# Performance work log

Hardware: AMD Instinct MI355X
Metric: run time of the kernel (lower is better)

The kernel has to match this reference:

```python
import jax, jax.numpy as jnp
import numpy as np

B, S, E, H = 4, 2048, 1024, 16
D = E // H  # head dim = 64


def setup_inputs() -> dict:
    key = jax.random.key(0)
    ks = jax.random.split(key, 5)
    s = 0.02
    return {
        "x": jax.random.normal(ks[0], (B, S, E), dtype=jnp.float32),
        "Wq": jax.random.normal(ks[1], (E, E), dtype=jnp.float32) * s,
        "Wk": jax.random.normal(ks[2], (E, E), dtype=jnp.float32) * s,
        "Wv": jax.random.normal(ks[3], (E, E), dtype=jnp.float32) * s,
        "Wo": jax.random.normal(ks[4], (E, E), dtype=jnp.float32) * s,
        "bo": jnp.zeros((E,), dtype=jnp.float32),
    }


def reference(x, Wq, Wk, Wv, Wo, bo):
    b, s, e = x.shape
    h, d = H, e // H
    # QKV projections -> [b, h, s, d]
    q = (x @ Wq).reshape(b, s, h, d).transpose(0, 2, 1, 3)
    k = (x @ Wk).reshape(b, s, h, d).transpose(0, 2, 1, 3)
    v = (x @ Wv).reshape(b, s, h, d).transpose(0, 2, 1, 3)
    # scores [b, h, s, s], causal mask with -inf, scaled softmax
    a = jnp.einsum('bhqd,bhkd->bhqk', q, k)
    causal = jnp.tril(jnp.ones((s, s), dtype=bool))  # True where allowed
    a = jnp.where(causal, a, -jnp.inf) / jnp.sqrt(jnp.asarray(d, x.dtype))
    a = jax.nn.softmax(a, axis=-1)
    # dropout p=0.0 (identity in eval)
    y = jnp.einsum('bhqk,bhkd->bhqd', a, v)
    y = y.transpose(0, 2, 1, 3).reshape(b, s, e)
    return y @ Wo + bo
```

## Files before the change

### kernel.cpp

```cpp
#include <hip/hip_runtime.h>

typedef __bf16 bf16x8 __attribute__((ext_vector_type(8)));
typedef float f32x4 __attribute__((ext_vector_type(4)));
typedef unsigned short u16x8 __attribute__((ext_vector_type(8)));

#define S_LEN 2048
#define NHEAD 16
#define HDIM  64
#define EMB   1024

__device__ __forceinline__ ushort f2b(float v) {
  union { float f; unsigned u; } x; x.f = v;
  unsigned r = (x.u + 0x7fffu + ((x.u >> 16) & 1u)) >> 16;
  return (ushort)r;
}

__device__ __forceinline__ ushort f2b_trunc(float v) {
  union { float f; unsigned u; } x; x.f = v;
  return (ushort)(x.u >> 16);
}

typedef const __attribute__((address_space(1))) unsigned int* gp1_t;
typedef __attribute__((address_space(3))) unsigned int* lp3_t;
__device__ __forceinline__ void gld16(const ushort* g, const ushort* l) {
  __builtin_amdgcn_global_load_lds((gp1_t)(unsigned long long)(uintptr_t)g,
                                   (lp3_t)(unsigned int)(uintptr_t)l, 16, 0, 0);
}

__device__ __forceinline__ void barf() {
  asm volatile("" ::: "memory");
  __builtin_amdgcn_s_barrier();
  asm volatile("" ::: "memory");
}

__global__ __launch_bounds__(256) void prep_kernel(
    const float* __restrict__ x, const float* __restrict__ W0,
    const float* __restrict__ W1, const float* __restrict__ W2,
    const float* __restrict__ W3, ushort* __restrict__ xb,
    ushort* __restrict__ Wt0, ushort* __restrict__ Wt1,
    ushort* __restrict__ Wt2, ushort* __restrict__ Wt3, float scale0) {
  const int z = blockIdx.z;
  if (z == 4) {
    size_t base = ((size_t)(blockIdx.y * 32 + blockIdx.x)) * 8192 + threadIdx.x * 4;
#pragma unroll
    for (int i = 0; i < 8; ++i) {
      float4 v = *(const float4*)(x + base + i * 1024);
      ushort4 o;
      o.x = f2b(v.x); o.y = f2b(v.y); o.z = f2b(v.z); o.w = f2b(v.w);
      *(ushort4*)(xb + base + i * 1024) = o;
    }
    return;
  }
  __shared__ float t[32][33];
  const float* W = z == 0 ? W0 : (z == 1 ? W1 : (z == 2 ? W2 : W3));
  ushort* Wt = z == 0 ? Wt0 : (z == 1 ? Wt1 : (z == 2 ? Wt2 : Wt3));
  const float scale = z == 0 ? scale0 : 1.0f;
  int k0 = blockIdx.x * 32, n0 = blockIdx.y * 32;
  int c = threadIdx.x & 31, r0 = threadIdx.x >> 5;
#pragma unroll
  for (int i = 0; i < 4; ++i) {
    int r = r0 + i * 8;
    t[r][c] = W[(size_t)(k0 + r) * EMB + n0 + c];
  }
  __syncthreads();
#pragma unroll
  for (int i = 0; i < 4; ++i) {
    int r = r0 + i * 8;
    Wt[(size_t)(n0 + r) * EMB + k0 + c] = f2b(t[c][r] * scale);
  }
}

template <int EPI>
__global__ __launch_bounds__(512, 2) void gemm8_kernel(
    const ushort* __restrict__ A, const ushort* __restrict__ Bt,
    ushort* __restrict__ outQ, ushort* __restrict__ outK, ushort* __restrict__ outVt,
    float* __restrict__ outF, const float* __restrict__ bias) {
  __shared__ ushort lds8[73728];
  const int tid = threadIdx.x;
  const int wave = tid >> 6, lane = tid & 63, ln = lane & 15, quad = lane >> 4;
  const int wm = wave >> 2, wn = wave & 3;
  const long m0 = (long)blockIdx.x * 128, n0 = (long)blockIdx.y * 256;
  constexpr int K = EMB, KT = K / 64;

  const int srow = tid >> 3;
  const int scol = ((tid & 7) ^ (srow & 7)) * 8;
  const ushort* srcA = A + (m0 + srow) * (long)K + scol;
  const ushort* srcB = Bt + (n0 + srow) * (long)K + scol;

#define STG_A(t, s)                                                            \
  do {                                                                         \
    gld16(srcA + (t) * 64,               lds8 + (s) * 8192 + tid * 8);         \
    gld16(srcA + (t) * 64 + 64 * K,      lds8 + (s) * 8192 + 4096 + tid * 8);  \
  } while (0)
#define STG_B(t, s)                                                            \
  do {                                                                         \
    gld16(srcB + (t) * 64,               lds8 + 24576 + (s) * 16384 + tid * 8);         \
    gld16(srcB + (t) * 64 + 64 * K,      lds8 + 24576 + (s) * 16384 + 4096 + tid * 8);  \
    gld16(srcB + (t) * 64 + 128 * K,     lds8 + 24576 + (s) * 16384 + 8192 + tid * 8);  \
    gld16(srcB + (t) * 64 + 192 * K,     lds8 + 24576 + (s) * 16384 + 12288 + tid * 8); \
  } while (0)

  const int sw = (ln & 7) * 8;

#define RD_A(F, kk, s)                                                         \
  do {                                                                         \
    const ushort* p_ = lds8 + (s) * 8192 + (wm * 64 + ln) * 64 +               \
                       (((kk) * 32 + quad * 8) ^ sw);                          \
    F[0] = *(const bf16x8*)p_;                                                 \
    F[1] = *(const bf16x8*)(p_ + 1024);                                        \
    F[2] = *(const bf16x8*)(p_ + 2048);                                        \
    F[3] = *(const bf16x8*)(p_ + 3072);                                        \
  } while (0)
#define RD_B(F, kk, s)                                                         \
  do {                                                                         \
    const ushort* p_ = lds8 + 24576 + (s) * 16384 + (wn * 64 + ln) * 64 +      \
                       (((kk) * 32 + quad * 8) ^ sw);                          \
    F[0] = *(const bf16x8*)p_;                                                 \
    F[1] = *(const bf16x8*)(p_ + 1024);                                        \
    F[2] = *(const bf16x8*)(p_ + 2048);                                        \
    F[3] = *(const bf16x8*)(p_ + 3072);                                        \
  } while (0)

#define MM16(AF, BF)                                                           \
  do {                                                                         \
    __builtin_amdgcn_s_setprio(1);                                             \
    _Pragma("unroll") for (int mt = 0; mt < 4; ++mt)                           \
        _Pragma("unroll") for (int nt = 0; nt < 4; ++nt)                       \
            acc[mt][nt] = __builtin_amdgcn_mfma_f32_16x16x32_bf16(             \
                AF[mt], BF[nt], acc[mt][nt], 0, 0, 0);                         \
    __builtin_amdgcn_s_setprio(0);                                             \
  } while (0)

  f32x4 acc[4][4] = {};
  bf16x8 afP[4], bfP[4], afN[4], bfN[4];

  STG_A(0, 0); STG_B(0, 0);
  STG_A(1, 1); STG_B(1, 1);
  asm volatile("s_waitcnt vmcnt(6)" ::: "memory");
  barf();
  RD_A(afP, 0, 0); RD_B(bfP, 0, 0);

#define TILE_FULL(t, s, s1, s2)                                                \
  do {                                                                         \
    STG_A((t) + 2, s2);                                                        \
    RD_A(afN, 1, s); RD_B(bfN, 1, s);                                          \
    MM16(afP, bfP);                               \
    STG_B((t) + 2, s2);                                                        \
    asm volatile("s_waitcnt vmcnt(6) lgkmcnt(0)" ::: "memory");                \
    barf();                               \
    RD_A(afP, 0, s1); RD_B(bfP, 0, s1);                        \
    MM16(afN, bfN);                               \
  } while (0)

  for (int th = 0; th < 12; th += 3) {
    TILE_FULL(th, 0, 1, 2);
    TILE_FULL(th + 1, 1, 2, 0);
    TILE_FULL(th + 2, 2, 0, 1);
  }
  TILE_FULL(12, 0, 1, 2);
  TILE_FULL(13, 1, 2, 0);
  RD_A(afN, 1, 2); RD_B(bfN, 1, 2);
  MM16(afP, bfP);
  asm volatile("s_waitcnt vmcnt(0) lgkmcnt(0)" ::: "memory");
  barf();
  RD_A(afP, 0, 0); RD_B(bfP, 0, 0);
  MM16(afN, bfN);
  RD_A(afN, 1, 0); RD_B(bfN, 1, 0);
  MM16(afP, bfP);
  MM16(afN, bfN);

  if (EPI == 0) {
    const int sel = (int)(n0 >> 10);
    if (sel == 2) {
#pragma unroll
      for (int mt = 0; mt < 4; ++mt) {
        const long mbase = m0 + wm * 64 + mt * 16 + quad * 4;
        const long bb = mbase >> 11, s = mbase & 2047;
#pragma unroll
        for (int nt = 0; nt < 4; ++nt) {
          const int nn = (int)((n0 & 1023) + wn * 64 + nt * 16 + ln);
          const int h = nn >> 6, d = nn & 63;
          uint2 val;
          val.x = (unsigned)f2b(acc[mt][nt][0]) | ((unsigned)f2b(acc[mt][nt][1]) << 16);
          val.y = (unsigned)f2b(acc[mt][nt][2]) | ((unsigned)f2b(acc[mt][nt][3]) << 16);
          *(uint2*)(outVt + (((bb * NHEAD + h) * (long)HDIM + d) * S_LEN) + s) = val;
        }
      }
    } else {
      ushort* dst = sel == 0 ? outQ : outK;
#pragma unroll
      for (int mt = 0; mt < 4; ++mt) {
#pragma unroll
        for (int nt = 0; nt < 4; ++nt) {
          const int nn = (int)((n0 & 1023) + wn * 64 + nt * 16 + ln);
          const int h = nn >> 6, d = nn & 63;
#pragma unroll
          for (int r = 0; r < 4; ++r) {
            const long m = m0 + wm * 64 + mt * 16 + quad * 4 + r;
            const long bb = m >> 11, s = m & 2047;
            dst[(((bb * NHEAD + h) * S_LEN) + s) * HDIM + d] = f2b(acc[mt][nt][r]);
          }
        }
      }
    }
  } else {
#pragma unroll
    for (int mt = 0; mt < 4; ++mt) {
#pragma unroll
      for (int nt = 0; nt < 4; ++nt) {
        const long n = n0 + wn * 64 + nt * 16 + ln;
        const float bv = bias[n];
#pragma unroll
        for (int r = 0; r < 4; ++r) {
          const long m = m0 + wm * 64 + mt * 16 + quad * 4 + r;
          outF[m * (long)EMB + n] = acc[mt][nt][r] + bv;
        }
      }
    }
  }
#undef TILE_FULL
#undef MM16
#undef RD_B
#undef RD_A
#undef STG_B
#undef STG_A
}

__global__ __launch_bounds__(256) void attn_kernel(const ushort* __restrict__ Q,
                                                   const ushort* __restrict__ Kg,
                                                   const ushort* __restrict__ Vt,
                                                   ushort* __restrict__ Y) {
  __shared__ alignas(16) ushort Ks[2][4096];
  __shared__ alignas(16) ushort Vs[2][4096];
  __shared__ alignas(16) ushort Ps[4 * 2 * 16 * 72];
  const int tid = threadIdx.x;
  const int wave = tid >> 6, lane = tid & 63, ln = lane & 15, quad = lane >> 4;
  const int bh = blockIdx.x;
  const int qb = 15 - (int)blockIdx.y;
  const int q0 = qb * 128;
  const size_t base = (size_t)bh * S_LEN * HDIM;
  const int ntiles = 2 * qb + 2;

  const u16x8 ob = {0x3F80, 0x3F80, 0x3F80, 0x3F80, 0x3F80, 0x3F80, 0x3F80, 0x3F80};
  const bf16x8 ones = __builtin_bit_cast(bf16x8, ob);

  bf16x8 qf[2][2];
#pragma unroll
  for (int mt = 0; mt < 2; ++mt)
#pragma unroll
    for (int ks2 = 0; ks2 < 2; ++ks2)
      qf[mt][ks2] = *(const bf16x8*)(Q + base + (size_t)(q0 + wave * 32 + mt * 16 + ln) * HDIM +
                                     ks2 * 32 + quad * 8);

  f32x4 acc[2][4] = {};
  f32x4 accl[2] = {};

  const int srow = tid >> 3;
  const int scc  = ((tid & 7) ^ (srow & 7)) * 8;
  const ushort* KgS = Kg + base + (size_t)srow * HDIM + scc;
  const ushort* VgS = Vt + base + (size_t)srow * S_LEN + scc;

  {
    gld16(KgS,                       &Ks[0][0] + tid * 8);
    gld16(KgS + 32 * HDIM,           &Ks[0][0] + 2048 + tid * 8);
    gld16(VgS,                       &Vs[0][0] + tid * 8);
    gld16(VgS + 32 * (size_t)S_LEN,  &Vs[0][0] + 2048 + tid * 8);
  }
  __syncthreads();

  ushort* Pw0 = Ps + wave * 2304;
  ushort* Pw1 = Pw0 + 1152;
  const int swW = (quad >> 1) << 4;
  const int swR = (ln >> 3) << 4;
  const int swL = (ln & 7) * 8;

  for (int kt = 0; kt < ntiles; ++kt) {
    const int cur = kt & 1;
    const int k0 = kt * 64;
    if (kt + 1 < ntiles) {
      const int nb = cur ^ 1;
      const size_t k1 = (size_t)(k0 + 64);
      gld16(KgS + k1 * HDIM,                  &Ks[nb][0] + tid * 8);
      gld16(KgS + (k1 + 32) * HDIM,           &Ks[nb][0] + 2048 + tid * 8);
      gld16(VgS + k1,                         &Vs[nb][0] + tid * 8);
      gld16(VgS + 32 * (size_t)S_LEN + k1,    &Vs[nb][0] + 2048 + tid * 8);
    }
    const ushort* Kc = &Ks[cur][0];
    const ushort* Vc = &Vs[cur][0];
    const int qbase = q0 + wave * 32;

    if (k0 < qbase + 32) {
      f32x4 s0[4] = {}, s1[4] = {};
#pragma unroll
      for (int ks2 = 0; ks2 < 2; ++ks2) {
#pragma unroll
        for (int nt = 0; nt < 4; ++nt) {
          bf16x8 bk = *(const bf16x8*)(Kc + (nt * 16 + ln) * 64 +
                                       ((ks2 * 32 + quad * 8) ^ swL));
          s0[nt] = __builtin_amdgcn_mfma_f32_16x16x32_bf16(qf[0][ks2], bk, s0[nt], 0, 0, 0);
          s1[nt] = __builtin_amdgcn_mfma_f32_16x16x32_bf16(qf[1][ks2], bk, s1[nt], 0, 0, 0);
        }
      }

      if (k0 + 63 > qbase) {
        const int rowq = qbase + quad * 4;
#pragma unroll
        for (int nt = 0; nt < 4; ++nt)
#pragma unroll
          for (int r = 0; r < 4; ++r) {
            const int key = k0 + nt * 16 + ln;
            if (key > rowq + r) s0[nt][r] = -3.0e38f;
            if (key > rowq + 16 + r) s1[nt][r] = -3.0e38f;
          }
      }

      asm volatile("" ::: "memory");
#pragma unroll
      for (int nt = 0; nt < 4; ++nt) {
#pragma unroll
        for (int r = 0; r < 4; ++r) {
          float p0 = __builtin_amdgcn_exp2f(s0[nt][r]);
          float p1 = __builtin_amdgcn_exp2f(s1[nt][r]);
          const int row = (quad * 4 + r) * 72;
          const int col = (nt * 16 + ln) ^ swW;
          Pw0[row + col] = f2b_trunc(p0);
          Pw1[row + col] = f2b_trunc(p1);
        }
      }
      asm volatile("" ::: "memory");

#pragma unroll
      for (int ks2 = 0; ks2 < 2; ++ks2) {
        const int rcol = (ks2 * 32 + quad * 8) ^ swR;
        bf16x8 ap0 = *(const bf16x8*)(Pw0 + ln * 72 + rcol);
        bf16x8 ap1 = *(const bf16x8*)(Pw1 + ln * 72 + rcol);
        accl[0] = __builtin_amdgcn_mfma_f32_16x16x32_bf16(ap0, ones, accl[0], 0, 0, 0);
        accl[1] = __builtin_amdgcn_mfma_f32_16x16x32_bf16(ap1, ones, accl[1], 0, 0, 0);
#pragma unroll
        for (int t2 = 0; t2 < 4; ++t2) {
          bf16x8 bv = *(const bf16x8*)(Vc + (t2 * 16 + ln) * 64 +
                                       ((ks2 * 32 + quad * 8) ^ swL));
          acc[0][t2] = __builtin_amdgcn_mfma_f32_16x16x32_bf16(ap0, bv, acc[0][t2], 0, 0, 0);
          acc[1][t2] = __builtin_amdgcn_mfma_f32_16x16x32_bf16(ap1, bv, acc[1][t2], 0, 0, 0);
        }
      }
    }
    __syncthreads();
  }

  const long b = bh >> 4;
  const int h = bh & 15;
#pragma unroll
  for (int mt = 0; mt < 2; ++mt) {
#pragma unroll
    for (int r = 0; r < 4; ++r) {
      float inv = 1.0f / accl[mt][r];
      const int qq = q0 + wave * 32 + mt * 16 + quad * 4 + r;
#pragma unroll
      for (int t2 = 0; t2 < 4; ++t2)
        Y[(((b * S_LEN + qq) * NHEAD) + h) * HDIM + t2 * 16 + ln] = f2b(acc[mt][t2][r] * inv);
    }
  }
}

extern "C" void kernel_launch(void* const* d_in, const int* in_sizes, int n_in,
                              void* d_out, int out_size, void* d_ws, size_t ws_size,
                              hipStream_t stream) {
  const float* x  = (const float*)d_in[0];
  const float* Wq = (const float*)d_in[1];
  const float* Wk = (const float*)d_in[2];
  const float* Wv = (const float*)d_in[3];
  const float* Wo = (const float*)d_in[4];
  const float* bo = (const float*)d_in[5];
  float* out = (float*)d_out;

  const size_t XE = (size_t)8192 * EMB;
  ushort* ws    = (ushort*)d_ws;
  ushort* xb    = ws;
  ushort* Wtqkv = xb + XE;
  ushort* Wto   = Wtqkv + 3 * 1048576;
  ushort* Qb    = Wto + 1048576;
  ushort* Kb    = Qb + XE;
  ushort* Vtb   = Kb + XE;
  ushort* Yb    = xb;

  const float SCALE_Q = 1.4426950408889634f / 8.0f;

  prep_kernel<<<dim3(32, 32, 5), 256, 0, stream>>>(
      x, Wq, Wk, Wv, Wo, xb, Wtqkv, Wtqkv + 1048576, Wtqkv + 2097152, Wto, SCALE_Q);

  gemm8_kernel<0><<<dim3(64, 12), 512, 0, stream>>>(xb, Wtqkv, Qb, Kb, Vtb,
                                                    nullptr, nullptr);
  attn_kernel<<<dim3(64, 16), 256, 0, stream>>>(Qb, Kb, Vtb, Yb);
  gemm8_kernel<1><<<dim3(64, 4), 512, 0, stream>>>(Yb, Wto, nullptr, nullptr,
                                                   nullptr, out, bo);
}
```

Before: 233.9 us.

## Use 32x32x16 MFMA with transposed scores and register-shuffled P, dropping LDS staging

Rewrites the attention inner loop to use 32x32x16 bf16 MFMAs. Scores are computed transposed (K as the A operand), so each lane holds probabilities that can be packed into bf16 pairs and exchanged between half-waves with __shfl_xor to form the A operand for the PV product. This removes the per-tile LDS write/read round trip for P and its shared buffer, and launch bounds now request 3 blocks per CU. In exchange it adds cross-lane shuffles and selects, and puts more pressure on registers.

```diff
diff --git a/kernel.cpp b/kernel.cpp
--- a/kernel.cpp
+++ b/kernel.cpp
@@ -2,7 +2,9 @@
 
 typedef __bf16 bf16x8 __attribute__((ext_vector_type(8)));
 typedef float f32x4 __attribute__((ext_vector_type(4)));
+typedef float f32x16 __attribute__((ext_vector_type(16)));
 typedef unsigned short u16x8 __attribute__((ext_vector_type(8)));
+typedef unsigned int u32x4 __attribute__((ext_vector_type(4)));
 
 #define S_LEN 2048
 #define NHEAD 16
@@ -18,6 +20,11 @@
 __device__ __forceinline__ ushort f2b_trunc(float v) {
   union { float f; unsigned u; } x; x.f = v;
   return (ushort)(x.u >> 16);
+}
+
+__device__ __forceinline__ unsigned pk2(float lo, float hi) {
+  union { float f; unsigned u; } a, b; a.f = lo; b.f = hi;
+  return (b.u & 0xffff0000u) | (a.u >> 16);
 }
 
 typedef const __attribute__((address_space(1))) unsigned int* gp1_t;
@@ -144,12 +151,12 @@
   do {                                                                         \
     STG_A((t) + 2, s2);                                                        \
     RD_A(afN, 1, s); RD_B(bfN, 1, s);                                          \
-    MM16(afP, bfP);                               \
+    MM16(afP, bfP);                                                            \
     STG_B((t) + 2, s2);                                                        \
     asm volatile("s_waitcnt vmcnt(6) lgkmcnt(0)" ::: "memory");                \
-    barf();                               \
-    RD_A(afP, 0, s1); RD_B(bfP, 0, s1);                        \
-    MM16(afN, bfN);                               \
+    barf();                                                                    \
+    RD_A(afP, 0, s1); RD_B(bfP, 0, s1);                                        \
+    MM16(afN, bfN);                                                            \
   } while (0)
 
   for (int th = 0; th < 12; th += 3) {
@@ -226,15 +233,15 @@
 #undef STG_A
 }
 
-__global__ __launch_bounds__(256) void attn_kernel(const ushort* __restrict__ Q,
-                                                   const ushort* __restrict__ Kg,
-                                                   const ushort* __restrict__ Vt,
-                                                   ushort* __restrict__ Y) {
+__global__ __launch_bounds__(256, 3) void attn_kernel(const ushort* __restrict__ Q,
+                                                      const ushort* __restrict__ Kg,
+                                                      const ushort* __restrict__ Vt,
+                                                      ushort* __restrict__ Y) {
   __shared__ alignas(16) ushort Ks[2][4096];
   __shared__ alignas(16) ushort Vs[2][4096];
-  __shared__ alignas(16) ushort Ps[4 * 2 * 16 * 72];
   const int tid = threadIdx.x;
-  const int wave = tid >> 6, lane = tid & 63, ln = lane & 15, quad = lane >> 4;
+  const int wave = tid >> 6, lane = tid & 63;
+  const int l31 = lane & 31, hi = lane >> 5;
   const int bh = blockIdx.x;
   const int qb = 15 - (int)blockIdx.y;
   const int q0 = qb * 128;
@@ -244,16 +251,13 @@
   const u16x8 ob = {0x3F80, 0x3F80, 0x3F80, 0x3F80, 0x3F80, 0x3F80, 0x3F80, 0x3F80};
   const bf16x8 ones = __builtin_bit_cast(bf16x8, ob);
 
-  bf16x8 qf[2][2];
-#pragma unroll
-  for (int mt = 0; mt < 2; ++mt)
-#pragma unroll
-    for (int ks2 = 0; ks2 < 2; ++ks2)
-      qf[mt][ks2] = *(const bf16x8*)(Q + base + (size_t)(q0 + wave * 32 + mt * 16 + ln) * HDIM +
-                                     ks2 * 32 + quad * 8);
-
-  f32x4 acc[2][4] = {};
-  f32x4 accl[2] = {};
+  bf16x8 qf[4];
+#pragma unroll
+  for (int dsub = 0; dsub < 4; ++dsub)
+    qf[dsub] = *(const bf16x8*)(Q + base + (size_t)(q0 + wave * 32 + l31) * HDIM +
+                                dsub * 16 + hi * 8);
+
+  f32x16 acc0 = {}, acc1 = {}, accl = {};
 
   const int srow = tid >> 3;
   const int scc  = ((tid & 7) ^ (srow & 7)) * 8;
@@ -268,11 +272,8 @@
   }
   __syncthreads();
 
-  ushort* Pw0 = Ps + wave * 2304;
-  ushort* Pw1 = Pw0 + 1152;
-  const int swW = (quad >> 1) << 4;
-  const int swR = (ln >> 3) << 4;
-  const int swL = (ln & 7) * 8;
+  const int swL = (lane & 7) * 8;
+  const int qbase = q0 + wave * 32;
 
   for (int kt = 0; kt < ntiles; ++kt) {
     const int cur = kt & 1;
@@ -287,63 +288,69 @@
     }
     const ushort* Kc = &Ks[cur][0];
     const ushort* Vc = &Vs[cur][0];
-    const int qbase = q0 + wave * 32;
 
     if (k0 < qbase + 32) {
-      f32x4 s0[4] = {}, s1[4] = {};
-#pragma unroll
-      for (int ks2 = 0; ks2 < 2; ++ks2) {
-#pragma unroll
-        for (int nt = 0; nt < 4; ++nt) {
-          bf16x8 bk = *(const bf16x8*)(Kc + (nt * 16 + ln) * 64 +
-                                       ((ks2 * 32 + quad * 8) ^ swL));
-          s0[nt] = __builtin_amdgcn_mfma_f32_16x16x32_bf16(qf[0][ks2], bk, s0[nt], 0, 0, 0);
-          s1[nt] = __builtin_amdgcn_mfma_f32_16x16x32_bf16(qf[1][ks2], bk, s1[nt], 0, 0, 0);
+      f32x16 sT0 = {}, sT1 = {};
+#pragma unroll
+      for (int dsub = 0; dsub < 4; ++dsub) {
+        const int c = (dsub * 16 + hi * 8) ^ swL;
+        bf16x8 kf0 = *(const bf16x8*)(Kc + l31 * 64 + c);
+        bf16x8 kf1 = *(const bf16x8*)(Kc + (32 + l31) * 64 + c);
+        sT0 = __builtin_amdgcn_mfma_f32_32x32x16_bf16(kf0, qf[dsub], sT0, 0, 0, 0);
+        sT1 = __builtin_amdgcn_mfma_f32_32x32x16_bf16(kf1, qf[dsub], sT1, 0, 0, 0);
+      }
+
+      if (k0 + 63 > qbase) {
+        const int rowq = qbase + l31;
+#pragma unroll
+        for (int r = 0; r < 16; ++r) {
+          const int key = k0 + ((r & 3) + 8 * (r >> 2)) + 4 * hi;
+          if (key > rowq) sT0[r] = -3.0e38f;
+          if (key + 32 > rowq) sT1[r] = -3.0e38f;
         }
       }
 
-      if (k0 + 63 > qbase) {
-        const int rowq = qbase + quad * 4;
-#pragma unroll
-        for (int nt = 0; nt < 4; ++nt)
-#pragma unroll
-          for (int r = 0; r < 4; ++r) {
-            const int key = k0 + nt * 16 + ln;
-            if (key > rowq + r) s0[nt][r] = -3.0e38f;
-            if (key > rowq + 16 + r) s1[nt][r] = -3.0e38f;
-          }
-      }
-
-      asm volatile("" ::: "memory");
-#pragma unroll
-      for (int nt = 0; nt < 4; ++nt) {
-#pragma unroll
-        for (int r = 0; r < 4; ++r) {
-          float p0 = __builtin_amdgcn_exp2f(s0[nt][r]);
-          float p1 = __builtin_amdgcn_exp2f(s1[nt][r]);
-          const int row = (quad * 4 + r) * 72;
-          const int col = (nt * 16 + ln) ^ swW;
-          Pw0[row + col] = f2b_trunc(p0);
-          Pw1[row + col] = f2b_trunc(p1);
-        }
-      }
-      asm volatile("" ::: "memory");
-
-#pragma unroll
-      for (int ks2 = 0; ks2 < 2; ++ks2) {
-        const int rcol = (ks2 * 32 + quad * 8) ^ swR;
-        bf16x8 ap0 = *(const bf16x8*)(Pw0 + ln * 72 + rcol);
-        bf16x8 ap1 = *(const bf16x8*)(Pw1 + ln * 72 + rcol);
-        accl[0] = __builtin_amdgcn_mfma_f32_16x16x32_bf16(ap0, ones, accl[0], 0, 0, 0);
-        accl[1] = __builtin_amdgcn_mfma_f32_16x16x32_bf16(ap1, ones, accl[1], 0, 0, 0);
-#pragma unroll
-        for (int t2 = 0; t2 < 4; ++t2) {
-          bf16x8 bv = *(const bf16x8*)(Vc + (t2 * 16 + ln) * 64 +
-                                       ((ks2 * 32 + quad * 8) ^ swL));
-          acc[0][t2] = __builtin_amdgcn_mfma_f32_16x16x32_bf16(ap0, bv, acc[0][t2], 0, 0, 0);
-          acc[1][t2] = __builtin_amdgcn_mfma_f32_16x16x32_bf16(ap1, bv, acc[1][t2], 0, 0, 0);
-        }
-      }
+      unsigned pw0[8], pw1[8];
+#pragma unroll
+      for (int i = 0; i < 8; ++i) {
+        pw0[i] = pk2(__builtin_amdgcn_exp2f(sT0[2 * i]),
+                     __builtin_amdgcn_exp2f(sT0[2 * i + 1]));
+        pw1[i] = pk2(__builtin_amdgcn_exp2f(sT1[2 * i]),
+                     __builtin_amdgcn_exp2f(sT1[2 * i + 1]));
+      }
+
+#define KEYBLK(PW, KSQ0)                                                       \
+  do {                                                                         \
+    const unsigned e0 = (unsigned)__shfl_xor((int)(hi ? PW[0] : PW[2]), 32, 64); \
+    const unsigned e1 = (unsigned)__shfl_xor((int)(hi ? PW[1] : PW[3]), 32, 64); \
+    const unsigned e2 = (unsigned)__shfl_xor((int)(hi ? PW[4] : PW[6]), 32, 64); \
+    const unsigned e3 = (unsigned)__shfl_xor((int)(hi ? PW[5] : PW[7]), 32, 64); \
+    u32x4 fwA, fwB;                                                            \
+    fwA[0] = hi ? e0 : PW[0]; fwA[1] = hi ? e1 : PW[1];                        \
+    fwA[2] = hi ? PW[2] : e0; fwA[3] = hi ? PW[3] : e1;                        \
+    fwB[0] = hi ? e2 : PW[4]; fwB[1] = hi ? e3 : PW[5];                        \
+    fwB[2] = hi ? PW[6] : e2; fwB[3] = hi ? PW[7] : e3;                        \
+    bf16x8 paA = __builtin_bit_cast(bf16x8, fwA);                              \
+    bf16x8 paB = __builtin_bit_cast(bf16x8, fwB);                              \
+    accl = __builtin_amdgcn_mfma_f32_32x32x16_bf16(paA, ones, accl, 0, 0, 0);  \
+    accl = __builtin_amdgcn_mfma_f32_32x32x16_bf16(paB, ones, accl, 0, 0, 0);  \
+    {                                                                          \
+      const int vcA = (((KSQ0)) * 16 + hi * 8) ^ swL;                          \
+      bf16x8 va0 = *(const bf16x8*)(Vc + l31 * 64 + vcA);                      \
+      bf16x8 va1 = *(const bf16x8*)(Vc + (32 + l31) * 64 + vcA);               \
+      acc0 = __builtin_amdgcn_mfma_f32_32x32x16_bf16(paA, va0, acc0, 0, 0, 0); \
+      acc1 = __builtin_amdgcn_mfma_f32_32x32x16_bf16(paA, va1, acc1, 0, 0, 0); \
+      const int vcB = (((KSQ0) + 1) * 16 + hi * 8) ^ swL;                      \
+      bf16x8 vb0 = *(const bf16x8*)(Vc + l31 * 64 + vcB);                      \
+      bf16x8 vb1 = *(const bf16x8*)(Vc + (32 + l31) * 64 + vcB);               \
+      acc0 = __builtin_amdgcn_mfma_f32_32x32x16_bf16(paB, vb0, acc0, 0, 0, 0); \
+      acc1 = __builtin_amdgcn_mfma_f32_32x32x16_bf16(paB, vb1, acc1, 0, 0, 0); \
+    }                                                                          \
+  } while (0)
+
+      KEYBLK(pw0, 0);
+      KEYBLK(pw1, 2);
+#undef KEYBLK
     }
     __syncthreads();
   }
@@ -351,15 +358,12 @@
   const long b = bh >> 4;
   const int h = bh & 15;
 #pragma unroll
-  for (int mt = 0; mt < 2; ++mt) {
-#pragma unroll
-    for (int r = 0; r < 4; ++r) {
-      float inv = 1.0f / accl[mt][r];
-      const int qq = q0 + wave * 32 + mt * 16 + quad * 4 + r;
-#pragma unroll
-      for (int t2 = 0; t2 < 4; ++t2)
-        Y[(((b * S_LEN + qq) * NHEAD) + h) * HDIM + t2 * 16 + ln] = f2b(acc[mt][t2][r] * inv);
-    }
+  for (int r = 0; r < 16; ++r) {
+    const float inv = 1.0f / accl[r];
+    const int qq = q0 + wave * 32 + ((r & 3) + 8 * (r >> 2)) + 4 * hi;
+    ushort* yp = Y + (((b * S_LEN + qq) * NHEAD) + h) * HDIM;
+    yp[l31]      = f2b(acc0[r] * inv);
+    yp[32 + l31] = f2b(acc1[r] * inv);
   }
 }
 
```

Measured after the change: 218.3 us. -6.7%, faster.
